# Kernel optimization log

Hardware: AMD Instinct MI355X
Metric: run time of the kernel (lower is better)

The kernel has to match this reference:

```python
import jax, jax.numpy as jnp
import numpy as np

LX, LY = 256, 256
K_CLASSES = 4
N_SWEEPS = 2
N_SITES = LX * LY

# 8-neighborhood offsets (Moore neighborhood), border handled by clipping
_OFFSETS = np.array([[-1, -1], [-1, 0], [-1, 1],
                     [0, -1],           [0, 1],
                     [1, -1],  [1, 0],  [1, 1]], dtype=np.int32)


def setup_inputs() -> dict:
    key = jax.random.key(0)
    k1, k2, k3, k4 = jax.random.split(key, 4)
    X_init = jax.random.randint(k1, (LX, LY), 0, K_CLASSES).astype(jnp.int32)
    perm = jax.random.permutation(k2, jnp.arange(N_SITES)).astype(jnp.int32)
    uniforms = jax.random.uniform(k3, (N_SWEEPS, N_SITES), dtype=jnp.float32)
    beta = jax.random.uniform(k4, (), dtype=jnp.float32) + 0.5  # Potts coupling
    return {"X_init": X_init, "perm": perm, "uniforms": uniforms,
            "beta": beta, "K": K_CLASSES}


def reference(X_init, perm, uniforms, beta, K):
    lx, ly = X_init.shape
    off = jnp.asarray(_OFFSETS)              # (8, 2)
    classes = jnp.arange(K)                  # (K,)

    def update_one_site(X, uv, r):
        u, v = jnp.unravel_index(uv, (lx, ly))
        uu = jnp.clip(u + off[:, 0], 0, lx - 1)   # (8,) neighbor rows
        vv = jnp.clip(v + off[:, 1], 0, ly - 1)   # (8,) neighbor cols
        neigh = X[uu, vv]                          # (8,) dynamic gather
        # Potts potential: p_k proportional to exp(beta * #{neighbors == k})
        counts = (neigh[None, :] == classes[:, None]).sum(axis=1)  # (K,)
        probs = jax.nn.softmax(beta * counts.astype(jnp.float32))  # (K,) sums to 1
        # inverse-CDF categorical sample, as in the original cumsum < r
        x_sample = jnp.count_nonzero(jnp.cumsum(probs) < r)
        return X.at[u, v].set(x_sample.astype(X.dtype))  # scatter write

    def one_sweep(X, rs):
        def body(Xc, inp):
            uv, r = inp
            return update_one_site(Xc, uv, r), None
        X, _ = jax.lax.scan(body, X, (perm, rs))
        return X, None

    X_final, _ = jax.lax.scan(one_sweep, X_init, uniforms)  # N_SWEEPS sweeps
    return X_final
```

## Files before the change

kernel.cpp:

```cpp
#include <hip/hip_runtime.h>
#include <math.h>

#define NSITES 65536
#define WIN 4096
#define NW 16
#define RMAX 32


__device__ __forceinline__ int agg_pos(int v, int* c, int vmax) {
  int pos = 0;
  const int lane = threadIdx.x & 63;
  for (int vv = 1; vv <= vmax; ++vv) {
    unsigned long long m = __ballot(v == vv);
    if (m) {
      int leader = __ffsll((long long)m) - 1;
      int base = 0;
      if (lane == leader) base = atomicAdd(&c[vv], (int)__popcll(m));
      base = __shfl(base, leader);
      if (v == vv) pos = base + (int)__popcll(m & ((1ull << lane) - 1ull));
    }
  }
  return pos;
}

__device__ __forceinline__ void do_update(unsigned char* cell,
                                          const unsigned int* cellw,
                                          const float4* ctab, unsigned uvv,
                                          float r) {
  const int u = uvv >> 8, v = (int)(uvv & 255u);
  const int um = u ? u - 1 : 0, up = u < 255 ? u + 1 : 255;
  const int vm = v ? v - 1 : 0, vp = v < 255 ? v + 1 : 255;
  const int cb = vm >> 2;
  const int sh0 = (vm & 3) << 3;
  const int shv = (v - vm) << 3;
  const int shp = (vp - vm) << 3;
  int acc = 0;
  {
    const unsigned int* rw = cellw + (um << 6) + cb;
    const unsigned long long wd =
        ((unsigned long long)rw[1] << 32) | (unsigned long long)rw[0];
    const unsigned wl = (unsigned)(wd >> sh0);
    acc += 1 << ((wl & 255u) << 2);
    acc += 1 << (((wl >> shv) & 255u) << 2);
    acc += 1 << (((wl >> shp) & 255u) << 2);
  }
  {
    const unsigned int* rw = cellw + (u << 6) + cb;
    const unsigned long long wd =
        ((unsigned long long)rw[1] << 32) | (unsigned long long)rw[0];
    const unsigned wl = (unsigned)(wd >> sh0);
    acc += 1 << ((wl & 255u) << 2);
    acc += 1 << (((wl >> shp) & 255u) << 2);
  }
  {
    const unsigned int* rw = cellw + (up << 6) + cb;
    const unsigned long long wd =
        ((unsigned long long)rw[1] << 32) | (unsigned long long)rw[0];
    const unsigned wl = (unsigned)(wd >> sh0);
    acc += 1 << ((wl & 255u) << 2);
    acc += 1 << (((wl >> shv) & 255u) << 2);
    acc += 1 << (((wl >> shp) & 255u) << 2);
  }
  const int n0 = acc & 15, n1 = (acc >> 4) & 15, n2 = (acc >> 8) & 15;
  const float4 c = ctab[n0 + 9 * n1 + 81 * n2];
  int cnt = (c.x < r) ? 1 : 0;
  cnt += (c.y < r) ? 1 : 0;
  cnt += (c.z < r) ? 1 : 0;
  cnt += (c.w < r) ? 1 : 0;
  cell[uvv] = (unsigned char)cnt;
}

__device__ __forceinline__ void run_rounds(unsigned char* cell,
                                           const unsigned int* cellw,
                                           const float4* ctab, const int* le,
                                           const uint2 (&R)[4], int tid) {
  int b = 0, e = le[1];
  for (int rd = 1; rd < RMAX; ++rd) {
    if (b >= WIN) break;
    const int nb = e;
    const int ne = (rd + 1 < RMAX) ? le[rd + 1] : e;
#pragma unroll
    for (int k = 0; k < 4; ++k) {
      const int s = tid + (k << 10);
      if (s >= b && s < e)
        do_update(cell, cellw, ctab, R[k].x, __uint_as_float(R[k].y));
    }
    __syncthreads();
    b = nb;
    e = ne;
  }
}

__global__ __launch_bounds__(1024) void GibbsSampler_90443421319469_kernel(
    const int* __restrict__ Xi, const int* __restrict__ perm,
    const float* __restrict__ uni, const float* __restrict__ betap,
    uint2* __restrict__ recpk, int* __restrict__ ends,
    int* __restrict__ flag, int* __restrict__ out) {
#pragma clang fp contract(off)
  __shared__ __align__(16) unsigned char smem[139552];
  unsigned short* posg = (unsigned short*)smem;
  unsigned short* lvl = (unsigned short*)(smem + 131072);
  int* cnt = (int*)(smem + 139264);
  int* coff = (int*)(smem + 139396);
  int* bmax = (int*)(smem + 139532);
  unsigned int* cellw = (unsigned int*)smem;
  float4* ctab = (float4*)(smem + 65536);
  int* lend = (int*)(smem + 77248);

  const int tid = threadIdx.x;
  const int w = blockIdx.x;
  const int wbase = w * WIN;

  for (int g = tid; g < NSITES / 8; g += 1024)
    ((uint4*)posg)[g] = make_uint4(0u, 0u, 0u, 0u);
  for (int i = tid; i <= RMAX; i += 1024) { cnt[i] = 0; coff[i] = 0; }
  if (tid == 0) *bmax = 0;
  __syncthreads();

  int uvk[4];
#pragma unroll
  for (int k = 0; k < 4; ++k) {
    const int lt = tid + k * 1024;
    uvk[k] = perm[wbase + lt];
    posg[uvk[k]] = (unsigned short)(lt + 1);
  }
  __syncthreads();

  unsigned short pred[4][8];
  int myl[4];
#pragma unroll
  for (int k = 0; k < 4; ++k) {
    const int lt = tid + k * 1024;
    const int uv = uvk[k], u = uv >> 8, v = uv & 255;
    const int um = u ? u - 1 : 0, up = u < 255 ? u + 1 : 255;
    const int vm = v ? v - 1 : 0, vp = v < 255 ? v + 1 : 255;
    const int nb8[8] = {(um << 8) | vm, (um << 8) | v, (um << 8) | vp,
                        (u << 8) | vm,                 (u << 8) | vp,
                        (up << 8) | vm, (up << 8) | v, (up << 8) | vp};
    bool hasp = false;
#pragma unroll
    for (int j = 0; j < 8; ++j) {
      const int p = posg[nb8[j]];
      pred[k][j] = (p && p - 1 < lt) ? (unsigned short)(p - 1)
                                     : (unsigned short)0xFFFF;
      hasp |= (pred[k][j] != (unsigned short)0xFFFF);
    }
    myl[k] = hasp ? 2 : 1;
    lvl[lt] = (unsigned short)myl[k];
  }
  __syncthreads();

  for (int pass = 1; pass < 128; ++pass) {
    bool ch = false;
#pragma unroll
    for (int k = 0; k < 4; ++k) {
      if (myl[k] > pass) {
        int m = 0;
#pragma unroll
        for (int j = 0; j < 8; ++j) {
          const unsigned short p = pred[k][j];
          if (p != 0xFFFF) m = max(m, (int)lvl[p]);
        }
        const int nl = m + 1;
        if (nl != myl[k]) {
          myl[k] = nl;
          lvl[tid + k * 1024] = (unsigned short)nl;
          ch = true;
        }
      }
    }
    if (__syncthreads_count((int)ch) == 0) break;
  }

#pragma unroll
  for (int k = 0; k < 4; ++k) atomicMax(bmax, myl[k]);
  __syncthreads();
  const int vmax = *bmax;

#pragma unroll
  for (int k = 0; k < 4; ++k) (void)agg_pos(myl[k], cnt, vmax);
  __syncthreads();
  if (tid == 0) {
    int e = 0;
    for (int r = 0; r < RMAX; ++r) {
      coff[r] = e;
      e += cnt[r];
      ends[w * RMAX + r] = e;
    }
  }
  __syncthreads();

#pragma unroll
  for (int k = 0; k < 4; ++k) {
    const int pos = agg_pos(myl[k], coff, vmax);
    const int lt = tid + k * 1024;
    const int gp = wbase + pos;
    recpk[gp] = make_uint2((unsigned)uvk[k],
                           __float_as_uint(uni[wbase + lt]));
    recpk[NSITES + gp] = make_uint2((unsigned)uvk[k],
                                    __float_as_uint(uni[NSITES + wbase + lt]));
  }
  __syncthreads();

  if (w != 0) {
    if (tid == 0) {
      __threadfence();
      atomicAdd(flag, 1);
    }
    return;
  }

  if (tid == 0) {
    while (__hip_atomic_load(flag, __ATOMIC_RELAXED,
                             __HIP_MEMORY_SCOPE_AGENT) < NW - 1)
      __builtin_amdgcn_s_sleep(2);
    __threadfence();
  }
  __syncthreads();

  unsigned char* cell = (unsigned char*)cellw;
  const float beta = betap[0];

  uint2 ra[4], rb[4];
#pragma unroll
  for (int k = 0; k < 4; ++k) ra[k] = recpk[tid + (k << 10)];

  for (int g = tid; g < NSITES / 4; g += 1024) {
    int4 x = ((const int4*)Xi)[g];
    cellw[g] = (unsigned)(x.x & 255) | ((unsigned)(x.y & 255) << 8) |
               ((unsigned)(x.z & 255) << 16) | ((unsigned)(x.w & 255) << 24);
  }
  if (tid < NW * RMAX) lend[tid] = ends[tid];
  for (int t = tid; t < 729; t += 1024) {
    const int n0 = t % 9, n1 = (t / 9) % 9, n2 = t / 81;
    const int n3 = 8 - n0 - n1 - n2;
    float4 val = make_float4(2.f, 2.f, 2.f, 2.f);
    if (n3 >= 0) {
      const int mx = max(max(n0, n1), max(n2, n3));
      const float xm = beta * (float)mx;
      const float x0 = beta * (float)n0;
      const float x1 = beta * (float)n1;
      const float x2 = beta * (float)n2;
      const float x3 = beta * (float)n3;
      const float e0 = (float)exp((double)(x0 - xm));
      const float e1 = (float)exp((double)(x1 - xm));
      const float e2 = (float)exp((double)(x2 - xm));
      const float e3 = (float)exp((double)(x3 - xm));
      const float s = ((e0 + e1) + e2) + e3;
      const float c0 = e0 / s;
      const float c1 = c0 + e1 / s;
      const float c2 = c1 + e2 / s;
      const float c3 = c2 + e3 / s;
      val = make_float4(c0, c1, c2, c3);
    }
    ctab[t] = val;
  }
  __syncthreads();

  for (int ww2 = 0; ww2 < 2 * NW; ++ww2) {
    const int ww = ww2 & (NW - 1);
    const int* le = &lend[ww * RMAX];
    const int wn = ww2 + 1;
    const uint2* rpn = recpk + (wn >> 4) * NSITES + (wn & (NW - 1)) * WIN;
    if ((ww2 & 1) == 0) {
      if (wn < 2 * NW) {
#pragma unroll
        for (int k = 0; k < 4; ++k) rb[k] = rpn[tid + (k << 10)];
      }
      run_rounds(cell, cellw, ctab, le, ra, tid);
    } else {
      if (wn < 2 * NW) {
#pragma unroll
        for (int k = 0; k < 4; ++k) ra[k] = rpn[tid + (k << 10)];
      }
      run_rounds(cell, cellw, ctab, le, rb, tid);
    }
  }

  for (int g = tid; g < NSITES / 4; g += 1024) {
    const unsigned p = cellw[g];
    int4 o;
    o.x = (int)(p & 255u);
    o.y = (int)((p >> 8) & 255u);
    o.z = (int)((p >> 16) & 255u);
    o.w = (int)((p >> 24) & 255u);
    ((int4*)out)[g] = o;
  }
}

extern "C" void kernel_launch(void* const* d_in, const int* in_sizes, int n_in,
                              void* d_out, int out_size, void* d_ws,
                              size_t ws_size, hipStream_t stream) {
  const int* Xi = (const int*)d_in[0];
  const int* perm = (const int*)d_in[1];
  const float* uni = (const float*)d_in[2];
  const float* beta = (const float*)d_in[3];
  int* out = (int*)d_out;

  char* ws = (char*)d_ws;
  uint2* recpk = (uint2*)ws;
  int* ends = (int*)(ws + 2 * NSITES * 8);
  int* flag = (int*)(ws + 2 * NSITES * 8 + NW * RMAX * 4);

  hipMemsetAsync(flag, 0, sizeof(int), stream);
  GibbsSampler_90443421319469_kernel<<<dim3(NW), dim3(1024), 0, stream>>>(
      Xi, perm, uni, beta, recpk, ends, flag, out);
}
```

Measured before the change: 212.6 us.

## Dedicate a separate block to the sequential sweep and split the CDF table

Launches NW+1 blocks so block 0 does no window-scheduling work and only runs the sequential Gibbs sweep. Block 0 now loads the grid and builds the CDF table while the other 16 blocks compute per-window level orders, and waits on the flag only afterwards. This overlaps setup with scheduling instead of serialising it behind window 0's analysis. The float4 CDF table is also split into two float2 arrays, trading one 16-byte LDS read for two 8-byte reads.

```diff
diff --git a/kernel.cpp b/kernel.cpp
--- a/kernel.cpp
+++ b/kernel.cpp
@@ -25,7 +25,8 @@
 
 __device__ __forceinline__ void do_update(unsigned char* cell,
                                           const unsigned int* cellw,
-                                          const float4* ctab, unsigned uvv,
+                                          const float2* ct01,
+                                          const float2* ct23, unsigned uvv,
                                           float r) {
   const int u = uvv >> 8, v = (int)(uvv & 255u);
   const int um = u ? u - 1 : 0, up = u < 255 ? u + 1 : 255;
@@ -62,17 +63,20 @@
     acc += 1 << (((wl >> shp) & 255u) << 2);
   }
   const int n0 = acc & 15, n1 = (acc >> 4) & 15, n2 = (acc >> 8) & 15;
-  const float4 c = ctab[n0 + 9 * n1 + 81 * n2];
-  int cnt = (c.x < r) ? 1 : 0;
-  cnt += (c.y < r) ? 1 : 0;
-  cnt += (c.z < r) ? 1 : 0;
-  cnt += (c.w < r) ? 1 : 0;
+  const int idx = n0 + 9 * n1 + 81 * n2;
+  const float2 a = ct01[idx];
+  const float2 b = ct23[idx];
+  int cnt = (a.x < r) ? 1 : 0;
+  cnt += (a.y < r) ? 1 : 0;
+  cnt += (b.x < r) ? 1 : 0;
+  cnt += (b.y < r) ? 1 : 0;
   cell[uvv] = (unsigned char)cnt;
 }
 
 __device__ __forceinline__ void run_rounds(unsigned char* cell,
                                            const unsigned int* cellw,
-                                           const float4* ctab, const int* le,
+                                           const float2* ct01,
+                                           const float2* ct23, const int* le,
                                            const uint2 (&R)[4], int tid) {
   int b = 0, e = le[1];
   for (int rd = 1; rd < RMAX; ++rd) {
@@ -83,7 +87,7 @@
     for (int k = 0; k < 4; ++k) {
       const int s = tid + (k << 10);
       if (s >= b && s < e)
-        do_update(cell, cellw, ctab, R[k].x, __uint_as_float(R[k].y));
+        do_update(cell, cellw, ct01, ct23, R[k].x, __uint_as_float(R[k].y));
     }
     __syncthreads();
     b = nb;
@@ -104,105 +108,107 @@
   int* coff = (int*)(smem + 139396);
   int* bmax = (int*)(smem + 139532);
   unsigned int* cellw = (unsigned int*)smem;
-  float4* ctab = (float4*)(smem + 65536);
-  int* lend = (int*)(smem + 77248);
+  float2* ct01 = (float2*)(smem + 65536);
+  float2* ct23 = (float2*)(smem + 71424);
+  int* lend = (int*)(smem + 77312);
 
   const int tid = threadIdx.x;
-  const int w = blockIdx.x;
-  const int wbase = w * WIN;
-
-  for (int g = tid; g < NSITES / 8; g += 1024)
-    ((uint4*)posg)[g] = make_uint4(0u, 0u, 0u, 0u);
-  for (int i = tid; i <= RMAX; i += 1024) { cnt[i] = 0; coff[i] = 0; }
-  if (tid == 0) *bmax = 0;
-  __syncthreads();
-
-  int uvk[4];
-#pragma unroll
-  for (int k = 0; k < 4; ++k) {
-    const int lt = tid + k * 1024;
-    uvk[k] = perm[wbase + lt];
-    posg[uvk[k]] = (unsigned short)(lt + 1);
-  }
-  __syncthreads();
-
-  unsigned short pred[4][8];
-  int myl[4];
-#pragma unroll
-  for (int k = 0; k < 4; ++k) {
-    const int lt = tid + k * 1024;
-    const int uv = uvk[k], u = uv >> 8, v = uv & 255;
-    const int um = u ? u - 1 : 0, up = u < 255 ? u + 1 : 255;
-    const int vm = v ? v - 1 : 0, vp = v < 255 ? v + 1 : 255;
-    const int nb8[8] = {(um << 8) | vm, (um << 8) | v, (um << 8) | vp,
-                        (u << 8) | vm,                 (u << 8) | vp,
-                        (up << 8) | vm, (up << 8) | v, (up << 8) | vp};
-    bool hasp = false;
-#pragma unroll
-    for (int j = 0; j < 8; ++j) {
-      const int p = posg[nb8[j]];
-      pred[k][j] = (p && p - 1 < lt) ? (unsigned short)(p - 1)
-                                     : (unsigned short)0xFFFF;
-      hasp |= (pred[k][j] != (unsigned short)0xFFFF);
-    }
-    myl[k] = hasp ? 2 : 1;
-    lvl[lt] = (unsigned short)myl[k];
-  }
-  __syncthreads();
-
-  for (int pass = 1; pass < 128; ++pass) {
-    bool ch = false;
+
+  if (blockIdx.x != 0) {
+    const int w = blockIdx.x - 1;
+    const int wbase = w * WIN;
+
+    for (int g = tid; g < NSITES / 8; g += 1024)
+      ((uint4*)posg)[g] = make_uint4(0u, 0u, 0u, 0u);
+    for (int i = tid; i <= RMAX; i += 1024) { cnt[i] = 0; coff[i] = 0; }
+    if (tid == 0) *bmax = 0;
+    __syncthreads();
+
+    int uvk[4];
 #pragma unroll
     for (int k = 0; k < 4; ++k) {
-      if (myl[k] > pass) {
-        int m = 0;
-#pragma unroll
-        for (int j = 0; j < 8; ++j) {
-          const unsigned short p = pred[k][j];
-          if (p != 0xFFFF) m = max(m, (int)lvl[p]);
+      const int lt = tid + k * 1024;
+      uvk[k] = perm[wbase + lt];
+      posg[uvk[k]] = (unsigned short)(lt + 1);
+    }
+    __syncthreads();
+
+    unsigned short pred[4][8];
+    int myl[4];
+#pragma unroll
+    for (int k = 0; k < 4; ++k) {
+      const int lt = tid + k * 1024;
+      const int uv = uvk[k], u = uv >> 8, v = uv & 255;
+      const int um = u ? u - 1 : 0, up = u < 255 ? u + 1 : 255;
+      const int vm = v ? v - 1 : 0, vp = v < 255 ? v + 1 : 255;
+      const int nb8[8] = {(um << 8) | vm, (um << 8) | v, (um << 8) | vp,
+                          (u << 8) | vm,                 (u << 8) | vp,
+                          (up << 8) | vm, (up << 8) | v, (up << 8) | vp};
+      bool hasp = false;
+#pragma unroll
+      for (int j = 0; j < 8; ++j) {
+        const int p = posg[nb8[j]];
+        pred[k][j] = (p && p - 1 < lt) ? (unsigned short)(p - 1)
+                                       : (unsigned short)0xFFFF;
+        hasp |= (pred[k][j] != (unsigned short)0xFFFF);
+      }
+      myl[k] = hasp ? 2 : 1;
+      lvl[lt] = (unsigned short)myl[k];
+    }
+    __syncthreads();
+
+    for (int pass = 1; pass < 128; ++pass) {
+      bool ch = false;
+#pragma unroll
+      for (int k = 0; k < 4; ++k) {
+        if (myl[k] > pass) {
+          int m = 0;
+#pragma unroll
+          for (int j = 0; j < 8; ++j) {
+            const unsigned short p = pred[k][j];
+            if (p != 0xFFFF) m = max(m, (int)lvl[p]);
+          }
+          const int nl = m + 1;
+          if (nl != myl[k]) {
+            myl[k] = nl;
+            lvl[tid + k * 1024] = (unsigned short)nl;
+            ch = true;
+          }
         }
-        const int nl = m + 1;
-        if (nl != myl[k]) {
-          myl[k] = nl;
-          lvl[tid + k * 1024] = (unsigned short)nl;
-          ch = true;
-        }
-      }
-    }
-    if (__syncthreads_count((int)ch) == 0) break;
-  }
-
-#pragma unroll
-  for (int k = 0; k < 4; ++k) atomicMax(bmax, myl[k]);
-  __syncthreads();
-  const int vmax = *bmax;
-
-#pragma unroll
-  for (int k = 0; k < 4; ++k) (void)agg_pos(myl[k], cnt, vmax);
-  __syncthreads();
-  if (tid == 0) {
-    int e = 0;
-    for (int r = 0; r < RMAX; ++r) {
-      coff[r] = e;
-      e += cnt[r];
-      ends[w * RMAX + r] = e;
-    }
-  }
-  __syncthreads();
-
-#pragma unroll
-  for (int k = 0; k < 4; ++k) {
-    const int pos = agg_pos(myl[k], coff, vmax);
-    const int lt = tid + k * 1024;
-    const int gp = wbase + pos;
-    recpk[gp] = make_uint2((unsigned)uvk[k],
-                           __float_as_uint(uni[wbase + lt]));
-    recpk[NSITES + gp] = make_uint2((unsigned)uvk[k],
-                                    __float_as_uint(uni[NSITES + wbase + lt]));
-  }
-  __syncthreads();
-
-  if (w != 0) {
+      }
+      if (__syncthreads_count((int)ch) == 0) break;
+    }
+
+#pragma unroll
+    for (int k = 0; k < 4; ++k) atomicMax(bmax, myl[k]);
+    __syncthreads();
+    const int vmax = *bmax;
+
+#pragma unroll
+    for (int k = 0; k < 4; ++k) (void)agg_pos(myl[k], cnt, vmax);
+    __syncthreads();
+    if (tid == 0) {
+      int e = 0;
+      for (int r = 0; r < RMAX; ++r) {
+        coff[r] = e;
+        e += cnt[r];
+        ends[w * RMAX + r] = e;
+      }
+    }
+    __syncthreads();
+
+#pragma unroll
+    for (int k = 0; k < 4; ++k) {
+      const int pos = agg_pos(myl[k], coff, vmax);
+      const int lt = tid + k * 1024;
+      const int gp = wbase + pos;
+      recpk[gp] = make_uint2((unsigned)uvk[k],
+                             __float_as_uint(uni[wbase + lt]));
+      recpk[NSITES + gp] =
+          make_uint2((unsigned)uvk[k],
+                     __float_as_uint(uni[NSITES + wbase + lt]));
+    }
+    __syncthreads();
     if (tid == 0) {
       __threadfence();
       atomicAdd(flag, 1);
@@ -210,27 +216,14 @@
     return;
   }
 
-  if (tid == 0) {
-    while (__hip_atomic_load(flag, __ATOMIC_RELAXED,
-                             __HIP_MEMORY_SCOPE_AGENT) < NW - 1)
-      __builtin_amdgcn_s_sleep(2);
-    __threadfence();
-  }
-  __syncthreads();
-
   unsigned char* cell = (unsigned char*)cellw;
   const float beta = betap[0];
-
-  uint2 ra[4], rb[4];
-#pragma unroll
-  for (int k = 0; k < 4; ++k) ra[k] = recpk[tid + (k << 10)];
 
   for (int g = tid; g < NSITES / 4; g += 1024) {
     int4 x = ((const int4*)Xi)[g];
     cellw[g] = (unsigned)(x.x & 255) | ((unsigned)(x.y & 255) << 8) |
                ((unsigned)(x.z & 255) << 16) | ((unsigned)(x.w & 255) << 24);
   }
-  if (tid < NW * RMAX) lend[tid] = ends[tid];
   for (int t = tid; t < 729; t += 1024) {
     const int n0 = t % 9, n1 = (t / 9) % 9, n2 = t / 81;
     const int n3 = 8 - n0 - n1 - n2;
@@ -253,8 +246,22 @@
       const float c3 = c2 + e3 / s;
       val = make_float4(c0, c1, c2, c3);
     }
-    ctab[t] = val;
-  }
+    ct01[t] = make_float2(val.x, val.y);
+    ct23[t] = make_float2(val.z, val.w);
+  }
+
+  if (tid == 0) {
+    while (__hip_atomic_load(flag, __ATOMIC_RELAXED,
+                             __HIP_MEMORY_SCOPE_AGENT) < NW)
+      __builtin_amdgcn_s_sleep(2);
+    __threadfence();
+  }
+  __syncthreads();
+
+  uint2 ra[4], rb[4];
+#pragma unroll
+  for (int k = 0; k < 4; ++k) ra[k] = recpk[tid + (k << 10)];
+  if (tid < NW * RMAX) lend[tid] = ends[tid];
   __syncthreads();
 
   for (int ww2 = 0; ww2 < 2 * NW; ++ww2) {
@@ -267,13 +274,13 @@
 #pragma unroll
         for (int k = 0; k < 4; ++k) rb[k] = rpn[tid + (k << 10)];
       }
-      run_rounds(cell, cellw, ctab, le, ra, tid);
+      run_rounds(cell, cellw, ct01, ct23, le, ra, tid);
     } else {
       if (wn < 2 * NW) {
 #pragma unroll
         for (int k = 0; k < 4; ++k) ra[k] = rpn[tid + (k << 10)];
       }
-      run_rounds(cell, cellw, ctab, le, rb, tid);
+      run_rounds(cell, cellw, ct01, ct23, le, rb, tid);
     }
   }
 
@@ -303,6 +310,6 @@
   int* flag = (int*)(ws + 2 * NSITES * 8 + NW * RMAX * 4);
 
   hipMemsetAsync(flag, 0, sizeof(int), stream);
-  GibbsSampler_90443421319469_kernel<<<dim3(NW), dim3(1024), 0, stream>>>(
+  GibbsSampler_90443421319469_kernel<<<dim3(NW + 1), dim3(1024), 0, stream>>>(
       Xi, perm, uni, beta, recpk, ends, flag, out);
 }
```

Measured after the change: 210.8 us, median of 2. Within noise of the previous version (-0.9%).
